# Optimization experiments

Measured on AMD Instinct MI355X. Metric: run time of the kernel, lower is better.

Reference implementation:

```python
import jax, jax.numpy as jnp
import numpy as np

B, S, R, Z, NLHS = 1024, 277, 76, 56, 24  # batch, seq_len, n_rules, z_size, n_lhs_symbols


def setup_inputs() -> dict:
    key = jax.random.key(0)
    k1, k2, k3, k4, k5, k6 = jax.random.split(key, 6)
    model_out_x = jax.random.normal(k1, (B, S, R), jnp.float32)
    mu = jax.random.normal(k2, (B, Z), jnp.float32)
    log_var = 0.1 * jax.random.normal(k3, (B, Z), jnp.float32)
    # one-hot targets over rules
    tgt_idx = jax.random.randint(k4, (B, S), 0, R)
    target_x = jax.nn.one_hot(tgt_idx, R, dtype=jnp.float32)
    # binary allowed-transition masks per LHS symbol
    masks = (jax.random.uniform(k5, (NLHS, R)) < 0.3).astype(jnp.float32)
    masks = masks.at[:, 0].set(1.0)  # ensure no all-zero mask row
    ind_to_lhs_ind = jax.random.randint(k6, (R,), 0, NLHS)
    return dict(model_out_x=model_out_x, mu=mu, log_var=log_var,
                target_x=target_x, masks=masks, ind_to_lhs_ind=ind_to_lhs_ind)


def reference(model_out_x, mu, log_var, target_x, masks, ind_to_lhs_ind):
    b = model_out_x.shape[0]
    seq_len = model_out_x.shape[1]
    z_size = mu.shape[1]

    # --- apply_masks: vectorized gather replacing the nested python loops ---
    true_rule = jnp.argmax(target_x, axis=-1)          # [B,S]
    lhs = ind_to_lhs_ind[true_rule]                    # [B,S]
    mask = masks[lhs]                                  # [B,S,R]
    shift_to_tiny = -100.0 + (model_out_x.min() - model_out_x.max())
    x = model_out_x + (1.0 - mask) * shift_to_tiny

    # --- softmax + BCE (torch BCELoss clamps log terms at -100) ---
    p = jax.nn.softmax(x, axis=-1)
    log_p = jnp.maximum(jnp.log(p), -100.0)
    log_1mp = jnp.maximum(jnp.log1p(-p), -100.0)
    bce = -jnp.mean(target_x * log_p + (1.0 - target_x) * log_1mp)
    BCE = seq_len * bce

    # --- moment-matching error on mu ---
    avg_mu = jnp.sum(mu, axis=0) / b                   # [Z]
    var = (mu.T @ mu) / b                              # [Z,Z]
    var_err = var - jnp.eye(z_size, dtype=mu.dtype)
    var_err = jnp.tanh(var_err) * var_err
    mom_err = jnp.sum(avg_mu * avg_mu) / z_size + jnp.sum(var_err) / (z_size * z_size)

    # sample_z=False, module in training mode -> loss = BCE + mom_err
    return BCE + mom_err
```

## Files before the change

### kernel.cpp

```cpp
#include <hip/hip_runtime.h>
#include <math.h>

#define BB    1024
#define SS    277
#define RR    76
#define ZZ    56
#define NLHS  24
#define NROWS (BB*SS)
#define ROWS_PER_BLOCK 256
#define NBLOCKS (NROWS/ROWS_PER_BLOCK)
#define V4_PER_ROW (RR/4)
#define BLK_ELEMS (ROWS_PER_BLOCK*RR)
#define TOTAL_ELEMS 21558272.0

static_assert(NROWS % ROWS_PER_BLOCK == 0, "rows divide blocks");
static_assert(RR % 4 == 0, "rows are whole float4s");

#define LN2F  0.69314718056f
#define NLN2F (-144.26950409f)

__global__ __launch_bounds__(256) void bce_kernel(
    const float* __restrict__ model,
    const float* __restrict__ target,
    const float* __restrict__ masks,
    const int*   __restrict__ ind_to_lhs,
    double* __restrict__ partials)
{
    __shared__ unsigned int  smb[NLHS*4];
    __shared__ unsigned char sm_idx[ROWS_PER_BLOCK];
    __shared__ int           sm_lhs[RR];
    __shared__ float         sm_red[4];

    const int tid = threadIdx.x;

    if (tid < NLHS*4) smb[tid] = 0u;
    sm_idx[tid] = 0;
    __syncthreads();

    for (int e = tid; e < NLHS*RR; e += 256) {
        const int lhs = e / RR;
        const int r   = e - lhs*RR;
        if (masks[e] > 0.5f)
            atomicOr(&smb[lhs*4 + (r >> 5)], 1u << (r & 31));
    }
    if (tid < RR) sm_lhs[tid] = ind_to_lhs[tid];

    const size_t blk_base = (size_t)blockIdx.x * BLK_ELEMS;

    {
        const float4* t4 = (const float4*)(target + blk_base);
        #pragma unroll
        for (int k = 0; k < V4_PER_ROW; ++k) {
            const int v4 = tid + k*256;
            const float4 t = t4[v4];
            int he = -1;
            const int e = v4*4;
            if (t.x > 0.5f) he = e;
            if (t.y > 0.5f) he = e+1;
            if (t.z > 0.5f) he = e+2;
            if (t.w > 0.5f) he = e+3;
            if (he >= 0) {
                const int row = he / RR;
                sm_idx[row] = (unsigned char)(he - row*RR);
            }
        }
    }
    __syncthreads();

    const int true_r = (int)sm_idx[tid];
    const int lhs    = sm_lhs[true_r];
    const unsigned int mw0 = smb[lhs*4 + 0];
    const unsigned int mw1 = smb[lhs*4 + 1];
    const unsigned int mw2 = smb[lhs*4 + 2];

    const float4* m4 = (const float4*)(model + blk_base + (size_t)tid * RR);
    float4 x[V4_PER_ROW];
    #pragma unroll
    for (int k = 0; k < V4_PER_ROW; ++k) x[k] = m4[k];

    float mx = -1e30f;
    #pragma unroll
    for (int k = 0; k < V4_PER_ROW; ++k) {
        #pragma unroll
        for (int c = 0; c < 4; ++c) {
            const int r = k*4 + c;
            const unsigned int mw = (r < 32) ? mw0 : ((r < 64) ? mw1 : mw2);
            float* xp = (&x[k].x) + c;
            const bool un = (mw >> (r & 31)) & 1u;
            const float xm = un ? *xp : -1e30f;
            *xp = xm;
            mx = fmaxf(mx, xm);
        }
    }

    float s = 0.f;
    #pragma unroll
    for (int k = 0; k < V4_PER_ROW; ++k) {
        #pragma unroll
        for (int c = 0; c < 4; ++c) {
            float* xp = (&x[k].x) + c;
            const float e = __expf(*xp - mx);
            *xp = e;
            s += e;
        }
    }

    const float inv = 1.f / s;
    float sum_l2 = 0.f;
    float p_true = 0.f;
    #pragma unroll
    for (int k = 0; k < V4_PER_ROW; ++k) {
        #pragma unroll
        for (int c = 0; c < 4; ++c) {
            const int r = k*4 + c;
            const float p  = (&x[k].x)[c] * inv;
            const float l2 = __log2f(1.f - p);
            sum_l2 += fmaxf(l2, NLN2F);
            if (r == true_r) p_true = p;
        }
    }
    float row_sum = LN2F * sum_l2;
    const float l1c_t = fmaxf(LN2F * __log2f(1.f - p_true), -100.f);
    const float lp_t  = fmaxf(__logf(p_true), -100.f);
    row_sum += lp_t - l1c_t;

    #pragma unroll
    for (int off = 32; off; off >>= 1) row_sum += __shfl_xor(row_sum, off, 64);
    if ((tid & 63) == 0) sm_red[tid >> 6] = row_sum;
    __syncthreads();
    if (tid == 0)
        partials[blockIdx.x] = (double)((sm_red[0] + sm_red[1]) + (sm_red[2] + sm_red[3]));
}

__global__ __launch_bounds__(256) void mom_kernel(
    const float* __restrict__ mu, double* __restrict__ out)
{
    const int j    = blockIdx.x;
    const int w    = threadIdx.x >> 6;
    const int lane = threadIdx.x & 63;
    __shared__ float sdot[4][64];
    __shared__ float ssum[4];

    const int i  = (lane < ZZ) ? lane : 0;
    float dot = 0.f, s1 = 0.f;
    const int b0 = 256*w;
    #pragma unroll 4
    for (int b = b0; b < b0 + 256; ++b) {
        const float c = mu[b*ZZ + j];
        const float a = mu[b*ZZ + i];
        dot = fmaf(a, c, dot);
        s1 += c;
    }
    sdot[w][lane] = dot;
    if (lane == 0) ssum[w] = s1;
    __syncthreads();

    if (w == 0) {
        float term = 0.f;
        if (lane < ZZ) {
            const float var = (sdot[0][lane] + sdot[1][lane] + sdot[2][lane] + sdot[3][lane]) * (1.f/BB);
            const float ve  = var - ((lane == j) ? 1.f : 0.f);
            term = tanhf(ve) * ve * (1.f/(ZZ*ZZ));
            if (lane == j) {
                const float am = (ssum[0] + ssum[1] + ssum[2] + ssum[3]) * (1.f/BB);
                term = fmaf(am*am, 1.f/ZZ, term);
            }
        }
        #pragma unroll
        for (int off = 32; off; off >>= 1) term += __shfl_xor(term, off, 64);
        if (lane == 0) out[j] = (double)term;
    }
}

__global__ __launch_bounds__(256) void final_kernel(
    const double* __restrict__ partials, float* __restrict__ out)
{
    __shared__ double sred[4];
    const int tid = threadIdx.x;
    double s = 0.0;
    for (int k = tid; k < NBLOCKS; k += 256) s += partials[k];
    double m = (tid < ZZ) ? partials[NBLOCKS + tid] : 0.0;
    double val = s * (-(double)SS / TOTAL_ELEMS) + m;
    #pragma unroll
    for (int off = 32; off; off >>= 1) val += __shfl_xor(val, off, 64);
    if ((tid & 63) == 0) sred[tid >> 6] = val;
    __syncthreads();
    if (tid == 0) out[0] = (float)((sred[0] + sred[1]) + (sred[2] + sred[3]));
}

extern "C" void kernel_launch(void* const* d_in, const int* in_sizes, int n_in,
                              void* d_out, int out_size, void* d_ws, size_t ws_size,
                              hipStream_t stream) {
    const float* model  = (const float*)d_in[0];
    const float* mu     = (const float*)d_in[1];
    const float* target = (const float*)d_in[3];
    const float* masks  = (const float*)d_in[4];
    const int*   ind    = (const int*)  d_in[5];
    float* out  = (float*)d_out;
    double* acc = (double*)d_ws;

    bce_kernel  <<<NBLOCKS, 256, 0, stream>>>(model, target, masks, ind, acc);
    mom_kernel  <<<ZZ,      256, 0, stream>>>(mu, acc + NBLOCKS);
    final_kernel<<<1,       256, 0, stream>>>(acc, out);
}
```

Measured before the change: 234.8 us.

## Stage model rows through LDS with coalesced loads, four threads per row, fuse mom kernel

Before, each thread loaded its own 76-float row directly from global memory, so the loads were strided and uncoalesced. Now each block handles 64 rows, loads them into shared memory with coalesced float4 reads, and splits each row across four threads that combine their max and sum with lane shuffles. The moment-matching kernel is folded into the same launch as extra blocks, which removes one kernel launch. In exchange the block uses about 19KB of shared memory, which may limit occupancy, and the number of blocks grows fourfold.

```diff
diff --git a/kernel.cpp b/kernel.cpp
--- a/kernel.cpp
+++ b/kernel.cpp
@@ -7,34 +7,74 @@
 #define ZZ    56
 #define NLHS  24
 #define NROWS (BB*SS)
-#define ROWS_PER_BLOCK 256
-#define NBLOCKS (NROWS/ROWS_PER_BLOCK)
-#define V4_PER_ROW (RR/4)
+#define ROWS_PER_BLOCK 64
+#define NBCE (NROWS/ROWS_PER_BLOCK)
+#define NMOM ZZ
+#define NBLK (NBCE + NMOM)
+#define V4_PER_BLOCK (ROWS_PER_BLOCK*RR/4)
 #define BLK_ELEMS (ROWS_PER_BLOCK*RR)
 #define TOTAL_ELEMS 21558272.0
 
 static_assert(NROWS % ROWS_PER_BLOCK == 0, "rows divide blocks");
-static_assert(RR % 4 == 0, "rows are whole float4s");
 
 #define LN2F  0.69314718056f
 #define NLN2F (-144.26950409f)
 
-__global__ __launch_bounds__(256) void bce_kernel(
+__global__ __launch_bounds__(256) void fused_kernel(
     const float* __restrict__ model,
     const float* __restrict__ target,
     const float* __restrict__ masks,
     const int*   __restrict__ ind_to_lhs,
+    const float* __restrict__ mu,
     double* __restrict__ partials)
 {
+    __shared__ float         sm_x[BLK_ELEMS];
     __shared__ unsigned int  smb[NLHS*4];
+    __shared__ int           sm_lhs[RR];
     __shared__ unsigned char sm_idx[ROWS_PER_BLOCK];
-    __shared__ int           sm_lhs[RR];
     __shared__ float         sm_red[4];
+    __shared__ float         sdot[4][64];
+    __shared__ float         ssum[4];
 
     const int tid = threadIdx.x;
 
+    if (blockIdx.x >= NBCE) {
+        const int j    = blockIdx.x - NBCE;
+        const int w    = tid >> 6;
+        const int lane = tid & 63;
+        const int i    = (lane < ZZ) ? lane : 0;
+        float dot = 0.f, s1 = 0.f;
+        const int b0 = 256*w;
+        #pragma unroll 4
+        for (int b = b0; b < b0 + 256; ++b) {
+            const float c = mu[b*ZZ + j];
+            const float a = mu[b*ZZ + i];
+            dot = fmaf(a, c, dot);
+            s1 += c;
+        }
+        sdot[w][lane] = dot;
+        if (lane == 0) ssum[w] = s1;
+        __syncthreads();
+        if (w == 0) {
+            float term = 0.f;
+            if (lane < ZZ) {
+                const float var = (sdot[0][lane]+sdot[1][lane]+sdot[2][lane]+sdot[3][lane]) * (1.f/BB);
+                const float ve  = var - ((lane == j) ? 1.f : 0.f);
+                term = tanhf(ve) * ve * (1.f/(ZZ*ZZ));
+                if (lane == j) {
+                    const float am = (ssum[0]+ssum[1]+ssum[2]+ssum[3]) * (1.f/BB);
+                    term = fmaf(am*am, 1.f/ZZ, term);
+                }
+            }
+            #pragma unroll
+            for (int off = 32; off; off >>= 1) term += __shfl_xor(term, off, 64);
+            if (lane == 0) partials[blockIdx.x] = (double)term;
+        }
+        return;
+    }
+
     if (tid < NLHS*4) smb[tid] = 0u;
-    sm_idx[tid] = 0;
+    if (tid < ROWS_PER_BLOCK) sm_idx[tid] = 0;
     __syncthreads();
 
     for (int e = tid; e < NLHS*RR; e += 256) {
@@ -48,81 +88,102 @@
     const size_t blk_base = (size_t)blockIdx.x * BLK_ELEMS;
 
     {
+        const float4* m4  = (const float4*)(model + blk_base);
+        float4*       sx4 = (float4*)sm_x;
+        #pragma unroll
+        for (int k = 0; k < 4; ++k) sx4[tid + 256*k] = m4[tid + 256*k];
+        if (tid < V4_PER_BLOCK - 1024) sx4[1024 + tid] = m4[1024 + tid];
+    }
+
+    {
         const float4* t4 = (const float4*)(target + blk_base);
         #pragma unroll
-        for (int k = 0; k < V4_PER_ROW; ++k) {
-            const int v4 = tid + k*256;
-            const float4 t = t4[v4];
-            int he = -1;
-            const int e = v4*4;
-            if (t.x > 0.5f) he = e;
-            if (t.y > 0.5f) he = e+1;
-            if (t.z > 0.5f) he = e+2;
-            if (t.w > 0.5f) he = e+3;
-            if (he >= 0) {
-                const int row = he / RR;
-                sm_idx[row] = (unsigned char)(he - row*RR);
+        for (int k = 0; k < 5; ++k) {
+            const int v4 = tid + 256*k;
+            if (v4 < V4_PER_BLOCK) {
+                const float4 t = t4[v4];
+                int he = -1;
+                const int e = v4*4;
+                if (t.x > 0.5f) he = e;
+                if (t.y > 0.5f) he = e+1;
+                if (t.z > 0.5f) he = e+2;
+                if (t.w > 0.5f) he = e+3;
+                if (he >= 0) {
+                    const int row = he / RR;
+                    sm_idx[row] = (unsigned char)(he - row*RR);
+                }
             }
         }
     }
     __syncthreads();
 
-    const int true_r = (int)sm_idx[tid];
+    const int row    = tid >> 2;
+    const int t      = tid & 3;
+    const int true_r = (int)sm_idx[row];
     const int lhs    = sm_lhs[true_r];
-    const unsigned int mw0 = smb[lhs*4 + 0];
-    const unsigned int mw1 = smb[lhs*4 + 1];
-    const unsigned int mw2 = smb[lhs*4 + 2];
-
-    const float4* m4 = (const float4*)(model + blk_base + (size_t)tid * RR);
-    float4 x[V4_PER_ROW];
-    #pragma unroll
-    for (int k = 0; k < V4_PER_ROW; ++k) x[k] = m4[k];
+    const unsigned int w0 = smb[lhs*4 + 0];
+    const unsigned int w1 = smb[lhs*4 + 1];
+    const unsigned int w2 = smb[lhs*4 + 2];
+
+    const float4* xr = (const float4*)(sm_x + row*RR);
+    float4 v[5];
 
     float mx = -1e30f;
     #pragma unroll
-    for (int k = 0; k < V4_PER_ROW; ++k) {
-        #pragma unroll
-        for (int c = 0; c < 4; ++c) {
-            const int r = k*4 + c;
-            const unsigned int mw = (r < 32) ? mw0 : ((r < 64) ? mw1 : mw2);
-            float* xp = (&x[k].x) + c;
-            const bool un = (mw >> (r & 31)) & 1u;
+    for (int k = 0; k < 5; ++k) {
+        const int c = t + 4*k;
+        float4 xv = (c < 19) ? xr[c] : make_float4(-1e30f,-1e30f,-1e30f,-1e30f);
+        #pragma unroll
+        for (int cc = 0; cc < 4; ++cc) {
+            const int r = c*4 + cc;
+            const unsigned int mw = (r < 32) ? w0 : ((r < 64) ? w1 : w2);
+            float* xp = (&xv.x) + cc;
+            const bool un = (r < RR) && ((mw >> (r & 31)) & 1u);
             const float xm = un ? *xp : -1e30f;
             *xp = xm;
             mx = fmaxf(mx, xm);
         }
-    }
+        v[k] = xv;
+    }
+    mx = fmaxf(mx, __shfl_xor(mx, 1, 64));
+    mx = fmaxf(mx, __shfl_xor(mx, 2, 64));
 
     float s = 0.f;
     #pragma unroll
-    for (int k = 0; k < V4_PER_ROW; ++k) {
-        #pragma unroll
-        for (int c = 0; c < 4; ++c) {
-            float* xp = (&x[k].x) + c;
+    for (int k = 0; k < 5; ++k) {
+        #pragma unroll
+        for (int cc = 0; cc < 4; ++cc) {
+            float* xp = (&v[k].x) + cc;
             const float e = __expf(*xp - mx);
             *xp = e;
             s += e;
         }
     }
-
+    s += __shfl_xor(s, 1, 64);
+    s += __shfl_xor(s, 2, 64);
     const float inv = 1.f / s;
+
     float sum_l2 = 0.f;
     float p_true = 0.f;
-    #pragma unroll
-    for (int k = 0; k < V4_PER_ROW; ++k) {
-        #pragma unroll
-        for (int c = 0; c < 4; ++c) {
-            const int r = k*4 + c;
-            const float p  = (&x[k].x)[c] * inv;
+    bool  owner  = false;
+    #pragma unroll
+    for (int k = 0; k < 5; ++k) {
+        const int c = t + 4*k;
+        #pragma unroll
+        for (int cc = 0; cc < 4; ++cc) {
+            const int r = c*4 + cc;
+            const float p  = (&v[k].x)[cc] * inv;
             const float l2 = __log2f(1.f - p);
             sum_l2 += fmaxf(l2, NLN2F);
-            if (r == true_r) p_true = p;
+            if (r == true_r) { p_true = p; owner = true; }
         }
     }
     float row_sum = LN2F * sum_l2;
-    const float l1c_t = fmaxf(LN2F * __log2f(1.f - p_true), -100.f);
-    const float lp_t  = fmaxf(__logf(p_true), -100.f);
-    row_sum += lp_t - l1c_t;
+    if (owner) {
+        const float l1c_t = fmaxf(LN2F * __log2f(1.f - p_true), -100.f);
+        const float lp_t  = fmaxf(__logf(p_true), -100.f);
+        row_sum += lp_t - l1c_t;
+    }
 
     #pragma unroll
     for (int off = 32; off; off >>= 1) row_sum += __shfl_xor(row_sum, off, 64);
@@ -130,46 +191,6 @@
     __syncthreads();
     if (tid == 0)
         partials[blockIdx.x] = (double)((sm_red[0] + sm_red[1]) + (sm_red[2] + sm_red[3]));
-}
-
-__global__ __launch_bounds__(256) void mom_kernel(
-    const float* __restrict__ mu, double* __restrict__ out)
-{
-    const int j    = blockIdx.x;
-    const int w    = threadIdx.x >> 6;
-    const int lane = threadIdx.x & 63;
-    __shared__ float sdot[4][64];
-    __shared__ float ssum[4];
-
-    const int i  = (lane < ZZ) ? lane : 0;
-    float dot = 0.f, s1 = 0.f;
-    const int b0 = 256*w;
-    #pragma unroll 4
-    for (int b = b0; b < b0 + 256; ++b) {
-        const float c = mu[b*ZZ + j];
-        const float a = mu[b*ZZ + i];
-        dot = fmaf(a, c, dot);
-        s1 += c;
-    }
-    sdot[w][lane] = dot;
-    if (lane == 0) ssum[w] = s1;
-    __syncthreads();
-
-    if (w == 0) {
-        float term = 0.f;
-        if (lane < ZZ) {
-            const float var = (sdot[0][lane] + sdot[1][lane] + sdot[2][lane] + sdot[3][lane]) * (1.f/BB);
-            const float ve  = var - ((lane == j) ? 1.f : 0.f);
-            term = tanhf(ve) * ve * (1.f/(ZZ*ZZ));
-            if (lane == j) {
-                const float am = (ssum[0] + ssum[1] + ssum[2] + ssum[3]) * (1.f/BB);
-                term = fmaf(am*am, 1.f/ZZ, term);
-            }
-        }
-        #pragma unroll
-        for (int off = 32; off; off >>= 1) term += __shfl_xor(term, off, 64);
-        if (lane == 0) out[j] = (double)term;
-    }
 }
 
 __global__ __launch_bounds__(256) void final_kernel(
@@ -178,8 +199,8 @@
     __shared__ double sred[4];
     const int tid = threadIdx.x;
     double s = 0.0;
-    for (int k = tid; k < NBLOCKS; k += 256) s += partials[k];
-    double m = (tid < ZZ) ? partials[NBLOCKS + tid] : 0.0;
+    for (int k = tid; k < NBCE; k += 256) s += partials[k];
+    double m = (tid < NMOM) ? partials[NBCE + tid] : 0.0;
     double val = s * (-(double)SS / TOTAL_ELEMS) + m;
     #pragma unroll
     for (int off = 32; off; off >>= 1) val += __shfl_xor(val, off, 64);
@@ -199,7 +220,6 @@
     float* out  = (float*)d_out;
     double* acc = (double*)d_ws;
 
-    bce_kernel  <<<NBLOCKS, 256, 0, stream>>>(model, target, masks, ind, acc);
-    mom_kernel  <<<ZZ,      256, 0, stream>>>(mu, acc + NBLOCKS);
-    final_kernel<<<1,       256, 0, stream>>>(acc, out);
+    fused_kernel<<<NBLK, 256, 0, stream>>>(model, target, masks, ind, mu, acc);
+    final_kernel<<<1,    256, 0, stream>>>(acc, out);
 }
```

New measurement: 222.6 us. -5.2%, faster.

## Fuse moment kernel into BCE kernel and shrink blocks to one wavefront

Applied to the files above, without the earlier changes.

Merges the mu moment-matching kernel into the BCE kernel: the first 56 blocks compute moment terms and the rest process 64-row BCE tiles. Blocks shrink from 256 to 64 threads, so the block-level shared reduction and its barrier go away and each block writes one wavefront sum. This removes one kernel launch and lets the small moment work overlap with BCE. In exchange each block rebuilds the mask bitmap and target index on its own, which is four times more setup, and the partials array grows four times for the final kernel to sum.

```diff
diff --git a/kernel.cpp b/kernel.cpp
--- a/kernel.cpp
+++ b/kernel.cpp
@@ -7,51 +7,82 @@
 #define ZZ    56
 #define NLHS  24
 #define NROWS (BB*SS)
-#define ROWS_PER_BLOCK 256
-#define NBLOCKS (NROWS/ROWS_PER_BLOCK)
-#define V4_PER_ROW (RR/4)
+#define ROWS_PER_BLOCK 64
+#define NBCE (NROWS/ROWS_PER_BLOCK)
+#define NMOM ZZ
+#define NBLK (NBCE + NMOM)
+#define V4_PER_BLOCK (ROWS_PER_BLOCK*RR/4)
 #define BLK_ELEMS (ROWS_PER_BLOCK*RR)
 #define TOTAL_ELEMS 21558272.0
 
 static_assert(NROWS % ROWS_PER_BLOCK == 0, "rows divide blocks");
-static_assert(RR % 4 == 0, "rows are whole float4s");
 
 #define LN2F  0.69314718056f
 #define NLN2F (-144.26950409f)
 
-__global__ __launch_bounds__(256) void bce_kernel(
+__global__ __launch_bounds__(64, 4) void fused_kernel(
     const float* __restrict__ model,
     const float* __restrict__ target,
     const float* __restrict__ masks,
     const int*   __restrict__ ind_to_lhs,
+    const float* __restrict__ mu,
     double* __restrict__ partials)
 {
     __shared__ unsigned int  smb[NLHS*4];
+    __shared__ int           sm_lhs[RR];
     __shared__ unsigned char sm_idx[ROWS_PER_BLOCK];
-    __shared__ int           sm_lhs[RR];
-    __shared__ float         sm_red[4];
 
     const int tid = threadIdx.x;
 
+    if (blockIdx.x < NMOM) {
+        const int j = blockIdx.x;
+        const int i = (tid < ZZ) ? tid : 0;
+        float dot = 0.f, s1 = 0.f;
+        #pragma unroll 8
+        for (int b = 0; b < BB; ++b) {
+            const float c = mu[b*ZZ + j];
+            const float a = mu[b*ZZ + i];
+            dot = fmaf(a, c, dot);
+            s1 += c;
+        }
+        float term = 0.f;
+        if (tid < ZZ) {
+            const float var = dot * (1.f/BB);
+            const float ve  = var - ((tid == j) ? 1.f : 0.f);
+            term = tanhf(ve) * ve * (1.f/(ZZ*ZZ));
+            if (tid == j) {
+                const float am = s1 * (1.f/BB);
+                term = fmaf(am*am, 1.f/ZZ, term);
+            }
+        }
+        #pragma unroll
+        for (int off = 32; off; off >>= 1) term += __shfl_xor(term, off, 64);
+        if (tid == 0) partials[blockIdx.x] = (double)term;
+        return;
+    }
+
+    const int bce_blk = blockIdx.x - NMOM;
+
     if (tid < NLHS*4) smb[tid] = 0u;
+    if (tid < NLHS*4 - 64) smb[64 + tid] = 0u;
     sm_idx[tid] = 0;
     __syncthreads();
 
-    for (int e = tid; e < NLHS*RR; e += 256) {
+    for (int e = tid; e < NLHS*RR; e += 64) {
         const int lhs = e / RR;
         const int r   = e - lhs*RR;
         if (masks[e] > 0.5f)
             atomicOr(&smb[lhs*4 + (r >> 5)], 1u << (r & 31));
     }
-    if (tid < RR) sm_lhs[tid] = ind_to_lhs[tid];
+    for (int i = tid; i < RR; i += 64) sm_lhs[i] = ind_to_lhs[i];
 
-    const size_t blk_base = (size_t)blockIdx.x * BLK_ELEMS;
+    const size_t blk_base = (size_t)bce_blk * BLK_ELEMS;
 
     {
         const float4* t4 = (const float4*)(target + blk_base);
         #pragma unroll
-        for (int k = 0; k < V4_PER_ROW; ++k) {
-            const int v4 = tid + k*256;
+        for (int k = 0; k < 19; ++k) {
+            const int v4 = tid + 64*k;
             const float4 t = t4[v4];
             int he = -1;
             const int e = v4*4;
@@ -74,13 +105,13 @@
     const unsigned int mw2 = smb[lhs*4 + 2];
 
     const float4* m4 = (const float4*)(model + blk_base + (size_t)tid * RR);
-    float4 x[V4_PER_ROW];
+    float4 x[19];
     #pragma unroll
-    for (int k = 0; k < V4_PER_ROW; ++k) x[k] = m4[k];
+    for (int k = 0; k < 19; ++k) x[k] = m4[k];
 
     float mx = -1e30f;
     #pragma unroll
-    for (int k = 0; k < V4_PER_ROW; ++k) {
+    for (int k = 0; k < 19; ++k) {
         #pragma unroll
         for (int c = 0; c < 4; ++c) {
             const int r = k*4 + c;
@@ -95,7 +126,7 @@
 
     float s = 0.f;
     #pragma unroll
-    for (int k = 0; k < V4_PER_ROW; ++k) {
+    for (int k = 0; k < 19; ++k) {
         #pragma unroll
         for (int c = 0; c < 4; ++c) {
             float* xp = (&x[k].x) + c;
@@ -109,7 +140,7 @@
     float sum_l2 = 0.f;
     float p_true = 0.f;
     #pragma unroll
-    for (int k = 0; k < V4_PER_ROW; ++k) {
+    for (int k = 0; k < 19; ++k) {
         #pragma unroll
         for (int c = 0; c < 4; ++c) {
             const int r = k*4 + c;
@@ -126,50 +157,7 @@
 
     #pragma unroll
     for (int off = 32; off; off >>= 1) row_sum += __shfl_xor(row_sum, off, 64);
-    if ((tid & 63) == 0) sm_red[tid >> 6] = row_sum;
-    __syncthreads();
-    if (tid == 0)
-        partials[blockIdx.x] = (double)((sm_red[0] + sm_red[1]) + (sm_red[2] + sm_red[3]));
-}
-
-__global__ __launch_bounds__(256) void mom_kernel(
-    const float* __restrict__ mu, double* __restrict__ out)
-{
-    const int j    = blockIdx.x;
-    const int w    = threadIdx.x >> 6;
-    const int lane = threadIdx.x & 63;
-    __shared__ float sdot[4][64];
-    __shared__ float ssum[4];
-
-    const int i  = (lane < ZZ) ? lane : 0;
-    float dot = 0.f, s1 = 0.f;
-    const int b0 = 256*w;
-    #pragma unroll 4
-    for (int b = b0; b < b0 + 256; ++b) {
-        const float c = mu[b*ZZ + j];
-        const float a = mu[b*ZZ + i];
-        dot = fmaf(a, c, dot);
-        s1 += c;
-    }
-    sdot[w][lane] = dot;
-    if (lane == 0) ssum[w] = s1;
-    __syncthreads();
-
-    if (w == 0) {
-        float term = 0.f;
-        if (lane < ZZ) {
-            const float var = (sdot[0][lane] + sdot[1][lane] + sdot[2][lane] + sdot[3][lane]) * (1.f/BB);
-            const float ve  = var - ((lane == j) ? 1.f : 0.f);
-            term = tanhf(ve) * ve * (1.f/(ZZ*ZZ));
-            if (lane == j) {
-                const float am = (ssum[0] + ssum[1] + ssum[2] + ssum[3]) * (1.f/BB);
-                term = fmaf(am*am, 1.f/ZZ, term);
-            }
-        }
-        #pragma unroll
-        for (int off = 32; off; off >>= 1) term += __shfl_xor(term, off, 64);
-        if (lane == 0) out[j] = (double)term;
-    }
+    if (tid == 0) partials[blockIdx.x] = (double)row_sum;
 }
 
 __global__ __launch_bounds__(256) void final_kernel(
@@ -178,8 +166,8 @@
     __shared__ double sred[4];
     const int tid = threadIdx.x;
     double s = 0.0;
-    for (int k = tid; k < NBLOCKS; k += 256) s += partials[k];
-    double m = (tid < ZZ) ? partials[NBLOCKS + tid] : 0.0;
+    for (int k = NMOM + tid; k < NBLK; k += 256) s += partials[k];
+    double m = (tid < NMOM) ? partials[tid] : 0.0;
     double val = s * (-(double)SS / TOTAL_ELEMS) + m;
     #pragma unroll
     for (int off = 32; off; off >>= 1) val += __shfl_xor(val, off, 64);
@@ -199,7 +187,6 @@
     float* out  = (float*)d_out;
     double* acc = (double*)d_ws;
 
-    bce_kernel  <<<NBLOCKS, 256, 0, stream>>>(model, target, masks, ind, acc);
-    mom_kernel  <<<ZZ,      256, 0, stream>>>(mu, acc + NBLOCKS);
-    final_kernel<<<1,       256, 0, stream>>>(acc, out);
+    fused_kernel<<<NBLK, ROWS_PER_BLOCK, 0, stream>>>(model, target, masks, ind, mu, acc);
+    final_kernel<<<1, 256, 0, stream>>>(acc, out);
 }
```

New measurement: 239.2 us. Within noise of the previous version (+1.9%).
